# Kernel tuning notes

Measured on AMD Instinct MI355X. Metric: run time of the kernel, lower is better.

Reference implementation:

```python
import jax, jax.numpy as jnp
import numpy as np

B, S, D, H = 4, 2048, 1024, 16
DK = D // H


def setup_inputs() -> dict:
    key = jax.random.key(0)
    kx, kq, kk, kv, ko = jax.random.split(key, 5)
    scale = D ** -0.5
    return {
        "x": jax.random.normal(kx, (B, S, D), dtype=jnp.float32),
        "W_q": jax.random.normal(kq, (D, D), dtype=jnp.float32) * scale,
        "W_k": jax.random.normal(kk, (D, D), dtype=jnp.float32) * scale,
        "W_v": jax.random.normal(kv, (D, D), dtype=jnp.float32) * scale,
        "W_o": jax.random.normal(ko, (D, D), dtype=jnp.float32) * scale,
    }


def reference(x, W_q, W_k, W_v, W_o):
    b, s, d = x.shape
    # projections: x @ W.T  (weights stored [out, in])
    def proj(W):
        return (x @ W.T).reshape(b, s, H, DK).transpose(0, 2, 1, 3)  # [b,h,s,dk]
    Q, K, V = proj(W_q), proj(W_k), proj(W_v)
    scores = jnp.einsum('bhqd,bhkd->bhqk', Q, K) * (DK ** -0.5)
    causal = jnp.tril(jnp.ones((s, s), dtype=bool))
    scores = jnp.where(causal, scores, -jnp.inf)
    attn = jax.nn.softmax(scores, axis=-1)
    out = jnp.einsum('bhqk,bhkd->bhqd', attn, V)  # [b,h,s,dk]
    out = out.transpose(0, 2, 1, 3).reshape(b, s, d)
    return out @ W_o.T
```

## Files before the change

kernel.cpp:

```cpp
#include <hip/hip_runtime.h>
#include <stdint.h>

#define B_ 4
#define S_ 2048
#define D_ 1024
#define H_ 16
#define DK_ 64
#define M_ (B_*S_)

typedef __attribute__((ext_vector_type(8))) short bhalf8;
typedef __attribute__((ext_vector_type(4))) short bhalf4;
typedef __attribute__((ext_vector_type(4))) float floatx4;
typedef unsigned short bfu;
typedef unsigned int u32;

__device__ __forceinline__ bfu f2bf(float f) {
  union { float f; u32 u; } v; v.f = f;
  u32 r = v.u + 0x7FFFu + ((v.u >> 16) & 1u);
  return (bfu)(r >> 16);
}

__device__ __forceinline__ u32 cvtpk(float a, float b) {
  u32 r;
  asm("v_cvt_pk_bf16_f32 %0, %1, %2" : "=v"(r) : "v"(a), "v"(b));
  return r;
}

__device__ __forceinline__ void gll16(const bfu* g, bfu* l) {
  __builtin_amdgcn_global_load_lds((__attribute__((address_space(1))) void*)g,
                                   (__attribute__((address_space(3))) void*)l,
                                   16, 0, 0);
}

__global__ void cvt_all(const float* __restrict__ x,  const float* __restrict__ wq,
                        const float* __restrict__ wk, const float* __restrict__ wv,
                        const float* __restrict__ wo, bfu* __restrict__ dst) {
  const size_t u = ((size_t)blockIdx.x * blockDim.x + threadIdx.x) * 4;
  const size_t XN = (size_t)M_ * D_;
  const float* src;
  if (u < XN) {
    src = x + u;
  } else {
    const size_t v = u - XN;
    const int wsel = (int)(v >> 20);
    const size_t off = v & ((size_t)(1u << 20) - 1);
    src = ((wsel == 0) ? wq : (wsel == 1) ? wk : (wsel == 2) ? wv : wo) + off;
  }
  float4 vv = *(const float4*)src;
  ushort4 o;
  o.x = f2bf(vv.x); o.y = f2bf(vv.y); o.z = f2bf(vv.z); o.w = f2bf(vv.w);
  *(ushort4*)(dst + u) = o;
}

__device__ __forceinline__ void gemm_core_2ph(const bfu* __restrict__ A,
                                              const bfu* __restrict__ Bw,
                                              bfu* smem,
                                              int m0, int bn0,
                                              floatx4 (&acc)[4][4])
{
  const int tid  = threadIdx.x;
  const int lane = tid & 63;
  const int g    = lane >> 4;
  const int i16  = lane & 15;
  const int w    = tid >> 6;
  const int wm   = w >> 1, wn = w & 1;

  const int lrow = lane >> 3;
  const int scol = ((lane & 7) ^ lrow) << 3;
  const bfu* As = A  + (size_t)(m0  + w * 32 + lrow) * D_ + scol;
  const bfu* Bs = Bw + (size_t)(bn0 + w * 32 + lrow) * D_ + scol;
  const int ldst = w * 4 * 512;

  auto STAGE = [&](int t) {
    bfu* base = smem + (t & 1) * 16384;
    const int k0 = t * 64;
#pragma unroll
    for (int j = 0; j < 4; ++j)
      gll16(As + (size_t)j * 8 * D_ + k0, base + ldst + j * 512);
#pragma unroll
    for (int j = 0; j < 4; ++j)
      gll16(Bs + (size_t)j * 8 * D_ + k0, base + 8192 + ldst + j * 512);
  };

  auto COMPUTE = [&](int t) {
    const char* aTc = (const char*)(smem + (t & 1) * 16384);
    const char* bTc = aTc + 16384;
    __builtin_amdgcn_s_setprio(1);
#pragma unroll
    for (int kb = 0; kb < 2; ++kb) {
      bhalf8 af[4], bf[4];
#pragma unroll
      for (int f = 0; f < 4; ++f) {
        int arow = wm * 64 + f * 16 + i16;
        af[f] = *(const bhalf8*)(aTc + arow * 128 + ((kb * 64 + g * 16) ^ ((arow & 7) << 4)));
        int brow = wn * 64 + f * 16 + i16;
        bf[f] = *(const bhalf8*)(bTc + brow * 128 + ((kb * 64 + g * 16) ^ ((brow & 7) << 4)));
      }
#pragma unroll
      for (int fm = 0; fm < 4; ++fm)
#pragma unroll
        for (int fn = 0; fn < 4; ++fn)
          acc[fm][fn] = __builtin_amdgcn_mfma_f32_16x16x32_bf16(af[fm], bf[fn], acc[fm][fn], 0, 0, 0);
    }
    __builtin_amdgcn_s_setprio(0);
  };

  STAGE(0);
  __syncthreads();
  for (int t = 0; t < 16; ++t) {
    if (t + 1 < 16) STAGE(t + 1);
    COMPUTE(t);
    __syncthreads();
  }
}

__global__ __launch_bounds__(256) void qkv_gemm(const bfu* __restrict__ xb,
                                                const bfu* __restrict__ wqkv,
                                                bfu* __restrict__ Qd,
                                                bfu* __restrict__ Kd,
                                                bfu* __restrict__ Vtd)
{
  __shared__ bfu smem[2 * 16384];
  const int bid = blockIdx.x;
  const int wi   = bid >> 3;
  const int xblk = wi >> 3;
  const int y    = ((bid & 7) << 3) | (wi & 7);
  const int m0   = y * 128;
  const int z    = xblk >> 3;
  const int n0   = (xblk & 7) * 128;
  const int bn0  = xblk * 128;

  floatx4 acc[4][4] = {};
  gemm_core_2ph(xb, wqkv, smem, m0, bn0, acc);

  bfu* dst = (z == 0) ? Qd : (z == 1) ? Kd : Vtd;
  const int lane = threadIdx.x & 63;
  const int g = lane >> 4, i16 = lane & 15;
  const int w = threadIdx.x >> 6, wm = w >> 1, wn = w & 1;
#pragma unroll
  for (int fm = 0; fm < 4; ++fm) {
#pragma unroll
    for (int fn = 0; fn < 4; ++fn) {
      int col = n0 + wn * 64 + fn * 16 + i16;
      int h = col >> 6, dk = col & 63;
#pragma unroll
      for (int r = 0; r < 4; ++r) {
        int mrow = m0 + wm * 64 + fm * 16 + g * 4 + r;
        int b = mrow >> 11, s = mrow & (S_ - 1);
        size_t idx = (z == 2)
            ? ((size_t)((b * H_ + h) * DK_ + dk)) * S_ + s
            : ((size_t)((b * H_ + h) * S_ + s)) * DK_ + dk;
        dst[idx] = f2bf(acc[fm][fn][r]);
      }
    }
  }
}

__global__ __launch_bounds__(256) void out_gemm(const bfu* __restrict__ Ab,
                                                const bfu* __restrict__ wob,
                                                float* __restrict__ out)
{
  __shared__ bfu smem[2 * 16384];
  const int bid = blockIdx.x;
  const int wi   = bid >> 3;
  const int xblk = wi >> 3;
  const int y    = ((bid & 7) << 3) | (wi & 7);
  const int m0   = y * 128;
  const int n0   = xblk * 128;

  floatx4 acc[4][4] = {};
  gemm_core_2ph(Ab, wob, smem, m0, n0, acc);

  const int lane = threadIdx.x & 63;
  const int g = lane >> 4, i16 = lane & 15;
  const int w = threadIdx.x >> 6, wm = w >> 1, wn = w & 1;
#pragma unroll
  for (int fm = 0; fm < 4; ++fm)
#pragma unroll
    for (int fn = 0; fn < 4; ++fn) {
      int col = n0 + wn * 64 + fn * 16 + i16;
#pragma unroll
      for (int r = 0; r < 4; ++r) {
        int mrow = m0 + wm * 64 + fm * 16 + g * 4 + r;
        out[(size_t)mrow * D_ + col] = acc[fm][fn][r];
      }
    }
}

template<int BUF>
__device__ __forceinline__ void attn_tile(const char* smem, int t, int ntw, int qr,
                                          int koff0, int koff1, const int (&voff)[4],
                                          bhalf8 qa0, bhalf8 qa1, int g, int i16,
                                          floatx4 (&ot)[4], float& mC2, float& lp)
{
  const float C2 = 0.125f * 1.44269504f;
  floatx4 sa[4] = {};
#pragma unroll
  for (int cb = 0; cb < 4; ++cb) {
    bhalf8 kf0 = *(const bhalf8*)(smem + BUF + cb * 2048 + koff0);
    bhalf8 kf1 = *(const bhalf8*)(smem + BUF + cb * 2048 + koff1);
    sa[cb] = __builtin_amdgcn_mfma_f32_16x16x32_bf16(kf0, qa0, sa[cb], 0, 0, 0);
    sa[cb] = __builtin_amdgcn_mfma_f32_16x16x32_bf16(kf1, qa1, sa[cb], 0, 0, 0);
  }
  if (t == ntw - 1) {
    const int kv0 = t * 64;
#pragma unroll
    for (int cb = 0; cb < 4; ++cb)
#pragma unroll
      for (int r = 0; r < 4; ++r)
        if (kv0 + cb * 16 + g * 4 + r > qr + i16) sa[cb][r] = -3.0e38f;
  }
  float pm = sa[0][0];
#pragma unroll
  for (int cb = 0; cb < 4; ++cb)
#pragma unroll
    for (int r = 0; r < 4; ++r)
      pm = fmaxf(pm, sa[cb][r]);
  pm = fmaxf(pm, __shfl_xor(pm, 16));
  pm = fmaxf(pm, __shfl_xor(pm, 32));
  const float pmC2 = pm * C2;
  if (!__all(pmC2 - mC2 <= 8.0f)) {
    const float nmax = fmaxf(mC2, pmC2);
    const float al = exp2f(mC2 - nmax);
    mC2 = nmax;
    lp *= al;
#pragma unroll
    for (int da = 0; da < 4; ++da)
#pragma unroll
      for (int r = 0; r < 4; ++r)
        ot[da][r] *= al;
  }
  const float nm = -mC2;
  u32 pk[8];
  float ps = 0.f;
#pragma unroll
  for (int cb = 0; cb < 4; ++cb) {
    float p0 = exp2f(__builtin_fmaf(sa[cb][0], C2, nm));
    float p1 = exp2f(__builtin_fmaf(sa[cb][1], C2, nm));
    float p2 = exp2f(__builtin_fmaf(sa[cb][2], C2, nm));
    float p3 = exp2f(__builtin_fmaf(sa[cb][3], C2, nm));
    ps += (p0 + p1) + (p2 + p3);
    pk[cb * 2]     = cvtpk(p0, p1);
    pk[cb * 2 + 1] = cvtpk(p2, p3);
  }
  lp += ps;
#pragma unroll
  for (int da = 0; da < 4; ++da) {
#pragma unroll
    for (int cb = 0; cb < 4; ++cb) {
      bhalf4 vf = *(const bhalf4*)(smem + BUF + voff[cb] + da * 2048);
      union { u32 u[2]; bhalf4 h; } pu;
      pu.u[0] = pk[cb * 2]; pu.u[1] = pk[cb * 2 + 1];
      ot[da] = __builtin_amdgcn_mfma_f32_16x16x16bf16_1k(vf, pu.h, ot[da], 0, 0, 0);
    }
  }
}

__global__ __launch_bounds__(512, 4) void attn_kernel(const bfu* __restrict__ Q,
                                                      const bfu* __restrict__ Kc,
                                                      const bfu* __restrict__ Vt,
                                                      bfu* __restrict__ Oc)
{
  __shared__ char smem[2 * 32768];
  const int tid = threadIdx.x;
  const int lane = tid & 63;
  const int w = tid >> 6;
  const int g = lane >> 4, i16 = lane & 15;
  const int sw = (i16 & 7) << 4;
  const int bh = blockIdx.x;
  const int y0 = blockIdx.y;

  const bfu* Qb = Q  + (size_t)bh * S_ * DK_;
  const bfu* Kb = Kc + (size_t)bh * S_ * DK_;
  const bfu* Vb = Vt + (size_t)bh * DK_ * S_;
  const int b = bh >> 4, h = bh & 15;

  const int srow = tid >> 3;
  const int scolb = (tid & 7) * 16;
  const bfu* kgp = Kb + srow * DK_ + (scolb >> 1);
  const bfu* vgp = Vb + (size_t)srow * S_ + (scolb >> 1);
  char* kld = smem + srow * 128 + (scolb ^ ((srow & 7) << 4));
  const int vsw = ((srow & 7) << 4) | (srow & 8);
  char* vld0 = smem + 8192 + srow * 128 + ((scolb    ) ^ vsw);
  char* vld1 = smem + 8192 + srow * 128 + ((scolb + 8) ^ vsw);

  const int koff0 = i16 * 128 + ((g * 16) ^ sw);
  const int koff1 = i16 * 128 + ((64 + g * 16) ^ sw);
  const int vswr = sw | (i16 & 8);
  int voff[4];
#pragma unroll
  for (int cb = 0; cb < 4; ++cb)
    voff[cb] = 8192 + i16 * 128 + ((cb * 32 + g * 8) ^ vswr);

  for (int pass = 0; pass < 2; ++pass) {
    const int y = pass ? (15 - y0) : y0;
    const int ntw = 2 * y + 1 + (w >> 2);
    const int qr = y * 128 + w * 16;
    const int npair = y + 1;

    bhalf8 qa0 = *(const bhalf8*)(Qb + (size_t)(qr + i16) * DK_ + g * 8);
    bhalf8 qa1 = *(const bhalf8*)(Qb + (size_t)(qr + i16) * DK_ + 32 + g * 8);

    floatx4 ot[4] = {};
    float mC2 = -1.0e30f;
    float lp  = 0.f;

    union { bhalf8 h8; bhalf4 h4[2]; } vu;
    bhalf8 ka, va, kb2, vb2;
    ka  = *(const bhalf8*)kgp;                  va  = *(const bhalf8*)vgp;
    kb2 = *(const bhalf8*)(kgp + 4096);         vb2 = *(const bhalf8*)(vgp + 64);
    *(bhalf8*)kld = ka;  vu.h8 = va;  *(bhalf4*)vld0 = vu.h4[0]; *(bhalf4*)vld1 = vu.h4[1];
    *(bhalf8*)(kld + 16384) = kb2; vu.h8 = vb2;
    *(bhalf4*)(vld0 + 16384) = vu.h4[0]; *(bhalf4*)(vld1 + 16384) = vu.h4[1];
    __syncthreads();

    for (int i = 0; ; ++i) {
      const int pa = 2 * i + 1;
      const bool morea = (pa < npair);
      if (morea) {
        ka  = *(const bhalf8*)(kgp + (size_t)(2 * pa)     * 4096);
        va  = *(const bhalf8*)(vgp + (2 * pa)     * 64);
        kb2 = *(const bhalf8*)(kgp + (size_t)(2 * pa + 1) * 4096);
        vb2 = *(const bhalf8*)(vgp + (2 * pa + 1) * 64);
      }
      {
        const int t0 = 4 * i;
        attn_tile<0>(smem, t0, ntw, qr, koff0, koff1, voff, qa0, qa1, g, i16, ot, mC2, lp);
        if (t0 + 1 < ntw)
          attn_tile<16384>(smem, t0 + 1, ntw, qr, koff0, koff1, voff, qa0, qa1, g, i16, ot, mC2, lp);
      }
      if (!morea) break;
      *(bhalf8*)(kld + 32768) = ka;  vu.h8 = va;
      *(bhalf4*)(vld0 + 32768) = vu.h4[0]; *(bhalf4*)(vld1 + 32768) = vu.h4[1];
      *(bhalf8*)(kld + 49152) = kb2; vu.h8 = vb2;
      *(bhalf4*)(vld0 + 49152) = vu.h4[0]; *(bhalf4*)(vld1 + 49152) = vu.h4[1];
      __syncthreads();

      const int pb = 2 * i + 2;
      const bool moreb = (pb < npair);
      if (moreb) {
        ka  = *(const bhalf8*)(kgp + (size_t)(2 * pb)     * 4096);
        va  = *(const bhalf8*)(vgp + (2 * pb)     * 64);
        kb2 = *(const bhalf8*)(kgp + (size_t)(2 * pb + 1) * 4096);
        vb2 = *(const bhalf8*)(vgp + (2 * pb + 1) * 64);
      }
      {
        const int t0 = 4 * i + 2;
        attn_tile<32768>(smem, t0, ntw, qr, koff0, koff1, voff, qa0, qa1, g, i16, ot, mC2, lp);
        if (t0 + 1 < ntw)
          attn_tile<49152>(smem, t0 + 1, ntw, qr, koff0, koff1, voff, qa0, qa1, g, i16, ot, mC2, lp);
      }
      if (!moreb) break;
      *(bhalf8*)kld = ka;  vu.h8 = va;
      *(bhalf4*)vld0 = vu.h4[0]; *(bhalf4*)vld1 = vu.h4[1];
      *(bhalf8*)(kld + 16384) = kb2; vu.h8 = vb2;
      *(bhalf4*)(vld0 + 16384) = vu.h4[0]; *(bhalf4*)(vld1 + 16384) = vu.h4[1];
      __syncthreads();
    }
    __syncthreads();

    float lt = lp;
    lt += __shfl_xor(lt, 16);
    lt += __shfl_xor(lt, 32);
    const float rl = 1.0f / lt;
    const size_t rowbase = (size_t)(b * S_ + qr + i16) * D_ + h * 64;
#pragma unroll
    for (int da = 0; da < 4; ++da) {
      union { u32 u[2]; uint2 v; } ov;
      ov.u[0] = cvtpk(ot[da][0] * rl, ot[da][1] * rl);
      ov.u[1] = cvtpk(ot[da][2] * rl, ot[da][3] * rl);
      *(uint2*)(Oc + rowbase + da * 16 + g * 4) = ov.v;
    }
  }
}

extern "C" void kernel_launch(void* const* d_in, const int* in_sizes, int n_in,
                              void* d_out, int out_size, void* d_ws, size_t ws_size,
                              hipStream_t stream)
{
  const float* x  = (const float*)d_in[0];
  const float* wq = (const float*)d_in[1];
  const float* wk = (const float*)d_in[2];
  const float* wv = (const float*)d_in[3];
  const float* wo = (const float*)d_in[4];

  bfu* xb  = (bfu*)d_ws;
  bfu* wqb = xb  + (size_t)M_ * D_;
  bfu* wob = wqb + (size_t)3 * D_ * D_;
  bfu* Qd  = wob + (size_t)D_ * D_;
  bfu* Kd  = Qd  + (size_t)M_ * D_;
  bfu* Vtd = Kd  + (size_t)M_ * D_;
  bfu* Ad  = Vtd + (size_t)M_ * D_;

  const size_t total = (size_t)M_ * D_ + 4 * (size_t)D_ * D_;
  cvt_all<<<(int)(total / 4 / 256), 256, 0, stream>>>(x, wq, wk, wv, wo, xb);

  qkv_gemm<<<1536, 256, 0, stream>>>(xb, wqb, Qd, Kd, Vtd);
  attn_kernel<<<dim3(B_ * H_, 8), 512, 0, stream>>>(Qd, Kd, Vtd, Ad);
  out_gemm<<<512, 256, 0, stream>>>(Ad, wob, (float*)d_out);
}
```

Baseline: 184.4 us.

## Switch attention to 32x32x16 MFMA with 4 waves per block and permlane32 swap

Attention kernel moves from 16x16 MFMA tiles to 32x32x16 bf16 MFMA. Each wave now owns 32 query rows, so a block has 4 waves (256 threads) instead of 8. P fragments are rearranged between lane halves with v_permlane32_swap instead of going through LDS, and the K/V LDS layout and swizzle are redone for 16-byte accesses. The intent is higher MFMA throughput and fewer LDS reads per FLOP, at the cost of more accumulator registers per wave and fewer waves to hide latency.

Result: slower. 216.5 us (+17.4%).

```diff
diff --git a/kernel.cpp b/kernel.cpp
--- a/kernel.cpp
+++ b/kernel.cpp
@@ -8,9 +8,10 @@
 #define DK_ 64
 #define M_ (B_*S_)
 
-typedef __attribute__((ext_vector_type(8))) short bhalf8;
-typedef __attribute__((ext_vector_type(4))) short bhalf4;
-typedef __attribute__((ext_vector_type(4))) float floatx4;
+typedef __attribute__((ext_vector_type(8)))  short bhalf8;
+typedef __attribute__((ext_vector_type(4)))  short bhalf4;
+typedef __attribute__((ext_vector_type(4)))  float floatx4;
+typedef __attribute__((ext_vector_type(16))) float floatx16;
 typedef unsigned short bfu;
 typedef unsigned int u32;
 
@@ -188,85 +189,97 @@
 }
 
 template<int BUF>
-__device__ __forceinline__ void attn_tile(const char* smem, int t, int ntw, int qr,
-                                          int koff0, int koff1, const int (&voff)[4],
-                                          bhalf8 qa0, bhalf8 qa1, int g, int i16,
-                                          floatx4 (&ot)[4], float& mC2, float& lp)
+__device__ __forceinline__ void attn_tile32(const char* smem, int t, int ntw, int qr,
+                                            const int (&off)[4],
+                                            const bhalf8 (&qa)[4], int l31, int hi,
+                                            floatx16 (&ot)[2], float& mC2, float& lp)
 {
   const float C2 = 0.125f * 1.44269504f;
-  floatx4 sa[4] = {};
-#pragma unroll
-  for (int cb = 0; cb < 4; ++cb) {
-    bhalf8 kf0 = *(const bhalf8*)(smem + BUF + cb * 2048 + koff0);
-    bhalf8 kf1 = *(const bhalf8*)(smem + BUF + cb * 2048 + koff1);
-    sa[cb] = __builtin_amdgcn_mfma_f32_16x16x32_bf16(kf0, qa0, sa[cb], 0, 0, 0);
-    sa[cb] = __builtin_amdgcn_mfma_f32_16x16x32_bf16(kf1, qa1, sa[cb], 0, 0, 0);
-  }
+  floatx16 sa[2] = {};
+#pragma unroll
+  for (int cb = 0; cb < 2; ++cb)
+#pragma unroll
+    for (int ks = 0; ks < 4; ++ks) {
+      bhalf8 kf = *(const bhalf8*)(smem + BUF + cb * 4096 + off[ks]);
+      sa[cb] = __builtin_amdgcn_mfma_f32_32x32x16_bf16(kf, qa[ks], sa[cb], 0, 0, 0);
+    }
   if (t == ntw - 1) {
     const int kv0 = t * 64;
-#pragma unroll
-    for (int cb = 0; cb < 4; ++cb)
-#pragma unroll
-      for (int r = 0; r < 4; ++r)
-        if (kv0 + cb * 16 + g * 4 + r > qr + i16) sa[cb][r] = -3.0e38f;
+    const int q = qr + l31;
+#pragma unroll
+    for (int cb = 0; cb < 2; ++cb)
+#pragma unroll
+      for (int r = 0; r < 16; ++r) {
+        int kv = kv0 + cb * 32 + (r & 3) + 8 * (r >> 2) + 4 * hi;
+        if (kv > q) sa[cb][r] = -3.0e38f;
+      }
   }
   float pm = sa[0][0];
 #pragma unroll
-  for (int cb = 0; cb < 4; ++cb)
-#pragma unroll
-    for (int r = 0; r < 4; ++r)
+  for (int cb = 0; cb < 2; ++cb)
+#pragma unroll
+    for (int r = 0; r < 16; ++r)
       pm = fmaxf(pm, sa[cb][r]);
-  pm = fmaxf(pm, __shfl_xor(pm, 16));
   pm = fmaxf(pm, __shfl_xor(pm, 32));
   const float pmC2 = pm * C2;
   if (!__all(pmC2 - mC2 <= 8.0f)) {
     const float nmax = fmaxf(mC2, pmC2);
     const float al = exp2f(mC2 - nmax);
-    mC2 = nmax;
-    lp *= al;
-#pragma unroll
-    for (int da = 0; da < 4; ++da)
-#pragma unroll
-      for (int r = 0; r < 4; ++r)
-        ot[da][r] *= al;
+    mC2 = nmax; lp *= al;
+#pragma unroll
+    for (int d = 0; d < 2; ++d)
+#pragma unroll
+      for (int r = 0; r < 16; ++r)
+        ot[d][r] *= al;
   }
   const float nm = -mC2;
-  u32 pk[8];
+  u32 W[2][8];
   float ps = 0.f;
 #pragma unroll
-  for (int cb = 0; cb < 4; ++cb) {
-    float p0 = exp2f(__builtin_fmaf(sa[cb][0], C2, nm));
-    float p1 = exp2f(__builtin_fmaf(sa[cb][1], C2, nm));
-    float p2 = exp2f(__builtin_fmaf(sa[cb][2], C2, nm));
-    float p3 = exp2f(__builtin_fmaf(sa[cb][3], C2, nm));
-    ps += (p0 + p1) + (p2 + p3);
-    pk[cb * 2]     = cvtpk(p0, p1);
-    pk[cb * 2 + 1] = cvtpk(p2, p3);
+  for (int cb = 0; cb < 2; ++cb) {
+    float p[16];
+#pragma unroll
+    for (int r = 0; r < 16; ++r) {
+      p[r] = exp2f(__builtin_fmaf(sa[cb][r], C2, nm));
+      ps += p[r];
+    }
+    u32 A0 = cvtpk(p[0],  p[1]),  A1 = cvtpk(p[2],  p[3]);
+    u32 B0 = cvtpk(p[4],  p[5]),  B1 = cvtpk(p[6],  p[7]);
+    u32 A2 = cvtpk(p[8],  p[9]),  A3 = cvtpk(p[10], p[11]);
+    u32 B2 = cvtpk(p[12], p[13]), B3 = cvtpk(p[14], p[15]);
+    asm volatile("v_permlane32_swap_b32 %0, %1" : "+v"(A0), "+v"(B0));
+    asm volatile("v_permlane32_swap_b32 %0, %1" : "+v"(A1), "+v"(B1));
+    asm volatile("v_permlane32_swap_b32 %0, %1" : "+v"(A2), "+v"(B2));
+    asm volatile("v_permlane32_swap_b32 %0, %1" : "+v"(A3), "+v"(B3));
+    W[cb][0] = A0; W[cb][1] = A1; W[cb][2] = B0; W[cb][3] = B1;
+    W[cb][4] = A2; W[cb][5] = A3; W[cb][6] = B2; W[cb][7] = B3;
   }
   lp += ps;
 #pragma unroll
-  for (int da = 0; da < 4; ++da) {
-#pragma unroll
-    for (int cb = 0; cb < 4; ++cb) {
-      bhalf4 vf = *(const bhalf4*)(smem + BUF + voff[cb] + da * 2048);
-      union { u32 u[2]; bhalf4 h; } pu;
-      pu.u[0] = pk[cb * 2]; pu.u[1] = pk[cb * 2 + 1];
-      ot[da] = __builtin_amdgcn_mfma_f32_16x16x16bf16_1k(vf, pu.h, ot[da], 0, 0, 0);
-    }
-  }
-}
-
-__global__ __launch_bounds__(512, 4) void attn_kernel(const bfu* __restrict__ Q,
-                                                      const bfu* __restrict__ Kc,
-                                                      const bfu* __restrict__ Vt,
-                                                      bfu* __restrict__ Oc)
+  for (int c = 0; c < 4; ++c) {
+    union { u32 u[4]; bhalf8 h; } pf;
+    pf.u[0] = W[c >> 1][(c & 1) * 4 + 0];
+    pf.u[1] = W[c >> 1][(c & 1) * 4 + 1];
+    pf.u[2] = W[c >> 1][(c & 1) * 4 + 2];
+    pf.u[3] = W[c >> 1][(c & 1) * 4 + 3];
+#pragma unroll
+    for (int dh = 0; dh < 2; ++dh) {
+      bhalf8 vf = *(const bhalf8*)(smem + BUF + 8192 + dh * 4096 + off[c]);
+      ot[dh] = __builtin_amdgcn_mfma_f32_32x32x16_bf16(vf, pf.h, ot[dh], 0, 0, 0);
+    }
+  }
+}
+
+__global__ __launch_bounds__(256) void attn_kernel(const bfu* __restrict__ Q,
+                                                   const bfu* __restrict__ Kc,
+                                                   const bfu* __restrict__ Vt,
+                                                   bfu* __restrict__ Oc)
 {
   __shared__ char smem[2 * 32768];
   const int tid = threadIdx.x;
   const int lane = tid & 63;
   const int w = tid >> 6;
-  const int g = lane >> 4, i16 = lane & 15;
-  const int sw = (i16 & 7) << 4;
+  const int l31 = lane & 31, hi = lane >> 5;
   const int bh = blockIdx.x;
   const int y0 = blockIdx.y;
 
@@ -275,102 +288,108 @@
   const bfu* Vb = Vt + (size_t)bh * DK_ * S_;
   const int b = bh >> 4, h = bh & 15;
 
-  const int srow = tid >> 3;
-  const int scolb = (tid & 7) * 16;
-  const bfu* kgp = Kb + srow * DK_ + (scolb >> 1);
-  const bfu* vgp = Vb + (size_t)srow * S_ + (scolb >> 1);
-  char* kld = smem + srow * 128 + (scolb ^ ((srow & 7) << 4));
-  const int vsw = ((srow & 7) << 4) | (srow & 8);
-  char* vld0 = smem + 8192 + srow * 128 + ((scolb    ) ^ vsw);
-  char* vld1 = smem + 8192 + srow * 128 + ((scolb + 8) ^ vsw);
-
-  const int koff0 = i16 * 128 + ((g * 16) ^ sw);
-  const int koff1 = i16 * 128 + ((64 + g * 16) ^ sw);
-  const int vswr = sw | (i16 & 8);
-  int voff[4];
-#pragma unroll
-  for (int cb = 0; cb < 4; ++cb)
-    voff[cb] = 8192 + i16 * 128 + ((cb * 32 + g * 8) ^ vswr);
+  int off[4];
+#pragma unroll
+  for (int x = 0; x < 4; ++x)
+    off[x] = l31 * 128 + ((((x << 1) | hi) ^ (lane & 7)) << 4);
+
+  const int srow = tid >> 2;
+  const int scq  = tid & 3;
+  const bfu* kgp = Kb + srow * DK_ + scq * 16;
+  const bfu* vgp = Vb + (size_t)srow * S_ + scq * 16;
+  const int swz = (srow & 7) << 4;
+  char* kld0 = smem + srow * 128 + ((scq * 32)      ^ swz);
+  char* kld1 = smem + srow * 128 + ((scq * 32 + 16) ^ swz);
+  char* vld0 = smem + 8192 + srow * 128 + ((scq * 32)      ^ swz);
+  char* vld1 = smem + 8192 + srow * 128 + ((scq * 32 + 16) ^ swz);
 
   for (int pass = 0; pass < 2; ++pass) {
     const int y = pass ? (15 - y0) : y0;
-    const int ntw = 2 * y + 1 + (w >> 2);
-    const int qr = y * 128 + w * 16;
+    const int ntw = 2 * y + (w >> 1) + 1;
+    const int qr = y * 128 + w * 32;
     const int npair = y + 1;
 
-    bhalf8 qa0 = *(const bhalf8*)(Qb + (size_t)(qr + i16) * DK_ + g * 8);
-    bhalf8 qa1 = *(const bhalf8*)(Qb + (size_t)(qr + i16) * DK_ + 32 + g * 8);
-
-    floatx4 ot[4] = {};
+    bhalf8 qa[4];
+#pragma unroll
+    for (int ks = 0; ks < 4; ++ks)
+      qa[ks] = *(const bhalf8*)(Qb + (size_t)(qr + l31) * DK_ + ks * 16 + 8 * hi);
+
+    floatx16 ot[2] = {};
     float mC2 = -1.0e30f;
     float lp  = 0.f;
 
-    union { bhalf8 h8; bhalf4 h4[2]; } vu;
-    bhalf8 ka, va, kb2, vb2;
-    ka  = *(const bhalf8*)kgp;                  va  = *(const bhalf8*)vgp;
-    kb2 = *(const bhalf8*)(kgp + 4096);         vb2 = *(const bhalf8*)(vgp + 64);
-    *(bhalf8*)kld = ka;  vu.h8 = va;  *(bhalf4*)vld0 = vu.h4[0]; *(bhalf4*)vld1 = vu.h4[1];
-    *(bhalf8*)(kld + 16384) = kb2; vu.h8 = vb2;
-    *(bhalf4*)(vld0 + 16384) = vu.h4[0]; *(bhalf4*)(vld1 + 16384) = vu.h4[1];
+    bhalf8 ka0, ka1, va0, va1, kb0, kb1, vb0, vb1;
+    ka0 = *(const bhalf8*)kgp;            ka1 = *(const bhalf8*)(kgp + 8);
+    va0 = *(const bhalf8*)vgp;            va1 = *(const bhalf8*)(vgp + 8);
+    kb0 = *(const bhalf8*)(kgp + 4096);   kb1 = *(const bhalf8*)(kgp + 4104);
+    vb0 = *(const bhalf8*)(vgp + 64);     vb1 = *(const bhalf8*)(vgp + 72);
+    *(bhalf8*)kld0 = ka0; *(bhalf8*)kld1 = ka1;
+    *(bhalf8*)vld0 = va0; *(bhalf8*)vld1 = va1;
+    *(bhalf8*)(kld0 + 16384) = kb0; *(bhalf8*)(kld1 + 16384) = kb1;
+    *(bhalf8*)(vld0 + 16384) = vb0; *(bhalf8*)(vld1 + 16384) = vb1;
     __syncthreads();
 
     for (int i = 0; ; ++i) {
       const int pa = 2 * i + 1;
       const bool morea = (pa < npair);
       if (morea) {
-        ka  = *(const bhalf8*)(kgp + (size_t)(2 * pa)     * 4096);
-        va  = *(const bhalf8*)(vgp + (2 * pa)     * 64);
-        kb2 = *(const bhalf8*)(kgp + (size_t)(2 * pa + 1) * 4096);
-        vb2 = *(const bhalf8*)(vgp + (2 * pa + 1) * 64);
+        const size_t ko = (size_t)(2 * pa) * 4096;
+        const int vo = 2 * pa * 64;
+        ka0 = *(const bhalf8*)(kgp + ko);        ka1 = *(const bhalf8*)(kgp + ko + 8);
+        va0 = *(const bhalf8*)(vgp + vo);        va1 = *(const bhalf8*)(vgp + vo + 8);
+        kb0 = *(const bhalf8*)(kgp + ko + 4096); kb1 = *(const bhalf8*)(kgp + ko + 4104);
+        vb0 = *(const bhalf8*)(vgp + vo + 64);   vb1 = *(const bhalf8*)(vgp + vo + 72);
       }
       {
         const int t0 = 4 * i;
-        attn_tile<0>(smem, t0, ntw, qr, koff0, koff1, voff, qa0, qa1, g, i16, ot, mC2, lp);
+        attn_tile32<0>(smem, t0, ntw, qr, off, qa, l31, hi, ot, mC2, lp);
         if (t0 + 1 < ntw)
-          attn_tile<16384>(smem, t0 + 1, ntw, qr, koff0, koff1, voff, qa0, qa1, g, i16, ot, mC2, lp);
+          attn_tile32<16384>(smem, t0 + 1, ntw, qr, off, qa, l31, hi, ot, mC2, lp);
       }
       if (!morea) break;
-      *(bhalf8*)(kld + 32768) = ka;  vu.h8 = va;
-      *(bhalf4*)(vld0 + 32768) = vu.h4[0]; *(bhalf4*)(vld1 + 32768) = vu.h4[1];
-      *(bhalf8*)(kld + 49152) = kb2; vu.h8 = vb2;
-      *(bhalf4*)(vld0 + 49152) = vu.h4[0]; *(bhalf4*)(vld1 + 49152) = vu.h4[1];
+      *(bhalf8*)(kld0 + 32768) = ka0; *(bhalf8*)(kld1 + 32768) = ka1;
+      *(bhalf8*)(vld0 + 32768) = va0; *(bhalf8*)(vld1 + 32768) = va1;
+      *(bhalf8*)(kld0 + 49152) = kb0; *(bhalf8*)(kld1 + 49152) = kb1;
+      *(bhalf8*)(vld0 + 49152) = vb0; *(bhalf8*)(vld1 + 49152) = vb1;
       __syncthreads();
 
       const int pb = 2 * i + 2;
       const bool moreb = (pb < npair);
       if (moreb) {
-        ka  = *(const bhalf8*)(kgp + (size_t)(2 * pb)     * 4096);
-        va  = *(const bhalf8*)(vgp + (2 * pb)     * 64);
-        kb2 = *(const bhalf8*)(kgp + (size_t)(2 * pb + 1) * 4096);
-        vb2 = *(const bhalf8*)(vgp + (2 * pb + 1) * 64);
+        const size_t ko = (size_t)(2 * pb) * 4096;
+        const int vo = 2 * pb * 64;
+        ka0 = *(const bhalf8*)(kgp + ko);        ka1 = *(const bhalf8*)(kgp + ko + 8);
+        va0 = *(const bhalf8*)(vgp + vo);        va1 = *(const bhalf8*)(vgp + vo + 8);
+        kb0 = *(const bhalf8*)(kgp + ko + 4096); kb1 = *(const bhalf8*)(kgp + ko + 4104);
+        vb0 = *(const bhalf8*)(vgp + vo + 64);   vb1 = *(const bhalf8*)(vgp + vo + 72);
       }
       {
         const int t0 = 4 * i + 2;
-        attn_tile<32768>(smem, t0, ntw, qr, koff0, koff1, voff, qa0, qa1, g, i16, ot, mC2, lp);
+        attn_tile32<32768>(smem, t0, ntw, qr, off, qa, l31, hi, ot, mC2, lp);
         if (t0 + 1 < ntw)
-          attn_tile<49152>(smem, t0 + 1, ntw, qr, koff0, koff1, voff, qa0, qa1, g, i16, ot, mC2, lp);
+          attn_tile32<49152>(smem, t0 + 1, ntw, qr, off, qa, l31, hi, ot, mC2, lp);
       }
       if (!moreb) break;
-      *(bhalf8*)kld = ka;  vu.h8 = va;
-      *(bhalf4*)vld0 = vu.h4[0]; *(bhalf4*)vld1 = vu.h4[1];
-      *(bhalf8*)(kld + 16384) = kb2; vu.h8 = vb2;
-      *(bhalf4*)(vld0 + 16384) = vu.h4[0]; *(bhalf4*)(vld1 + 16384) = vu.h4[1];
+      *(bhalf8*)kld0 = ka0; *(bhalf8*)kld1 = ka1;
+      *(bhalf8*)vld0 = va0; *(bhalf8*)vld1 = va1;
+      *(bhalf8*)(kld0 + 16384) = kb0; *(bhalf8*)(kld1 + 16384) = kb1;
+      *(bhalf8*)(vld0 + 16384) = vb0; *(bhalf8*)(vld1 + 16384) = vb1;
       __syncthreads();
     }
     __syncthreads();
 
-    float lt = lp;
-    lt += __shfl_xor(lt, 16);
-    lt += __shfl_xor(lt, 32);
+    float lt = lp + __shfl_xor(lp, 32);
     const float rl = 1.0f / lt;
-    const size_t rowbase = (size_t)(b * S_ + qr + i16) * D_ + h * 64;
-#pragma unroll
-    for (int da = 0; da < 4; ++da) {
-      union { u32 u[2]; uint2 v; } ov;
-      ov.u[0] = cvtpk(ot[da][0] * rl, ot[da][1] * rl);
-      ov.u[1] = cvtpk(ot[da][2] * rl, ot[da][3] * rl);
-      *(uint2*)(Oc + rowbase + da * 16 + g * 4) = ov.v;
-    }
+    const size_t rowbase = (size_t)(b * S_ + qr + l31) * D_ + h * 64;
+#pragma unroll
+    for (int dh = 0; dh < 2; ++dh)
+#pragma unroll
+      for (int q4 = 0; q4 < 4; ++q4) {
+        union { u32 u[2]; uint2 v; } ov;
+        ov.u[0] = cvtpk(ot[dh][q4 * 4 + 0] * rl, ot[dh][q4 * 4 + 1] * rl);
+        ov.u[1] = cvtpk(ot[dh][q4 * 4 + 2] * rl, ot[dh][q4 * 4 + 3] * rl);
+        *(uint2*)(Oc + rowbase + dh * 32 + q4 * 8 + 4 * hi) = ov.v;
+      }
   }
 }
 
@@ -396,6 +415,6 @@
   cvt_all<<<(int)(total / 4 / 256), 256, 0, stream>>>(x, wq, wk, wv, wo, xb);
 
   qkv_gemm<<<1536, 256, 0, stream>>>(xb, wqb, Qd, Kd, Vtd);
-  attn_kernel<<<dim3(B_ * H_, 8), 512, 0, stream>>>(Qd, Kd, Vtd, Ad);
+  attn_kernel<<<dim3(B_ * H_, 8), 256, 0, stream>>>(Qd, Kd, Vtd, Ad);
   out_gemm<<<512, 256, 0, stream>>>(Ad, wob, (float*)d_out);
 }
```
